# Kernel tuning notes

Hardware: AMD Instinct MI355X
Metric: run time of the kernel (lower is better)

## Reference

```python
import jax, jax.numpy as jnp
import numpy as np

B, S, D, H, ROT = 2, 2048, 2048, 16, 64
HD = D // H  # 128


def setup_inputs() -> dict:
    key = jax.random.key(0)
    ks = jax.random.split(key, 6)
    sc = 0.02
    return {
        "hidden_states": jax.random.normal(ks[0], (B, S, D), jnp.float32),
        "attention_mask": jnp.zeros((B, 1, 1, S), jnp.float32),  # HF additive mask; 0 == keep
        "position_ids": jnp.tile(jnp.arange(S, dtype=jnp.int32), (B, 1)),
        "Wq": jax.random.normal(ks[1], (D, D), jnp.float32) * sc,
        "Wk": jax.random.normal(ks[2], (D, D), jnp.float32) * sc,
        "Wv": jax.random.normal(ks[3], (D, D), jnp.float32) * sc,
        "Wo": jax.random.normal(ks[4], (D, D), jnp.float32) * sc,
        "norm_const": 0.5 * jnp.ones((1, H, 1, 1), jnp.float32),
    }


def _rotate_every_two(x):
    x1 = x[..., ::2]
    x2 = x[..., 1::2]
    return jnp.stack((-x2, x1), axis=-1).reshape(x.shape)


def _apply_rope(x, sin, cos):
    # x: [B,S,H,ROT]; sin/cos: [B,S,ROT//2] -> repeat_interleave(2) as in GPT-J
    sin2 = jnp.repeat(sin, 2, axis=-1)[:, :, None, :]
    cos2 = jnp.repeat(cos, 2, axis=-1)[:, :, None, :]
    return x * cos2 + _rotate_every_two(x) * sin2


def reference(hidden_states, attention_mask, position_ids, Wq, Wk, Wv, Wo, norm_const):
    # projections (nn.Linear, no bias): y = x @ W^T
    q = (hidden_states @ Wq.T).reshape(B, S, H, HD)
    k = (hidden_states @ Wk.T).reshape(B, S, H, HD)
    v = (hidden_states @ Wv.T).reshape(B, S, H, HD).transpose(0, 2, 1, 3)  # [B,H,S,HD]

    # GPT-J sinusoidal rotary on first ROT dims
    inv_freq = 1.0 / (10000.0 ** (jnp.arange(0, ROT, 2, dtype=jnp.float32) / ROT))
    ang = position_ids.astype(jnp.float32)[:, :, None] * inv_freq  # [B,S,ROT//2]
    sin, cos = jnp.sin(ang), jnp.cos(ang)
    q = jnp.concatenate([_apply_rope(q[..., :ROT], sin, cos), q[..., ROT:]], axis=-1)
    k = jnp.concatenate([_apply_rope(k[..., :ROT], sin, cos), k[..., ROT:]], axis=-1)
    q = q.transpose(0, 2, 1, 3)  # [B,H,S,HD]
    k = k.transpose(0, 2, 1, 3)

    # cosine attention: L2-normalize q and k (F.normalize, eps=1e-12)
    eps = 1e-12
    qn = q / jnp.clip(jnp.linalg.norm(q, axis=-1, keepdims=True), eps)
    kn = k / jnp.clip(jnp.linalg.norm(k, axis=-1, keepdims=True), eps)

    keep = attention_mask == 0                               # [B,1,1,S] bool
    causal = jnp.tril(jnp.ones((S, S), bool))[None, None]    # [1,1,S,S]
    # per-query count of visible keys -> value rescale with learned exponent
    counts = jnp.sum((causal & keep).astype(jnp.float32), axis=-1, keepdims=True)  # [B,1,S,1]
    expo = jax.nn.sigmoid(norm_const)                        # [1,H,1,1]
    v = v / jnp.clip(counts ** expo, 1.0)                    # [B,H,S,HD]

    keep_t = jnp.swapaxes(keep, -1, -2).astype(q.dtype)      # [B,1,S,1]
    qn = qn * keep_t
    kn = kn * keep_t
    v = v * keep_t

    attn = jnp.einsum('bhqd,bhkd->bhqk', qn, kn)             # cosine scores
    attn = jnp.where(causal, attn, 0.0)                      # causal zero-mask (no softmax)
    out = jnp.einsum('bhqk,bhkd->bhqd', attn, v)             # [B,H,S,HD]
    out = out.transpose(0, 2, 1, 3).reshape(B, S, D)
    return out @ Wo.T
```

## Files before the change

kernel.cpp:

```cpp
#include <hip/hip_runtime.h>
#include <hip/hip_bf16.h>

typedef __attribute__((ext_vector_type(8))) short bf16x8;
typedef __attribute__((ext_vector_type(4))) float f32x4;
typedef unsigned short u16;
typedef unsigned int u32;

constexpr int B = 2, S = 2048, D = 2048, H = 16, HD = 128, ROT = 64;
constexpr int NQKV = 3 * D;

__device__ __forceinline__ void gload16(const u16* g, u16* l)
{
    __builtin_amdgcn_global_load_lds((const __attribute__((address_space(1))) void*)g,
                                     (__attribute__((address_space(3))) void*)l, 16, 0, 0);
}

__device__ __forceinline__ float bf2f(u32 lo16) { return __uint_as_float(lo16 << 16); }

__global__ void cast_kernel(const float* __restrict__ in, u16* __restrict__ out, int n4)
{
    int idx = blockIdx.x * blockDim.x + threadIdx.x;
    int stride = gridDim.x * blockDim.x;
    for (int i = idx; i < n4; i += stride) {
        float4 v = ((const float4*)in)[i];
        __hip_bfloat16 a = __float2bfloat16(v.x);
        __hip_bfloat16 b = __float2bfloat16(v.y);
        __hip_bfloat16 c = __float2bfloat16(v.z);
        __hip_bfloat16 d = __float2bfloat16(v.w);
        ushort4 o;
        o.x = *(u16*)&a; o.y = *(u16*)&b; o.z = *(u16*)&c; o.w = *(u16*)&d;
        ((ushort4*)out)[i] = o;
    }
}

__global__ void prep_kernel(const float* __restrict__ mask, const int* __restrict__ pos,
                            const float* __restrict__ ncst,
                            float* __restrict__ sinb, float* __restrict__ cosb,
                            float* __restrict__ keep, float* __restrict__ expo)
{
    int gid = blockIdx.x * blockDim.x + threadIdx.x;
    int total = B * S * 32;
    if (gid < total) {
        int j = gid & 31;
        int bs = gid >> 5;
        float p = (float)pos[bs];
        float f = powf(10000.f, -(float)j / 32.f);
        float ang = p * f;
        sinb[gid] = sinf(ang);
        cosb[gid] = cosf(ang);
        if (j == 0) keep[bs] = (mask[bs] == 0.f) ? 1.f : 0.f;
    }
    if (gid < H) expo[gid] = 1.f / (1.f + expf(-ncst[gid]));
}

__global__ void counts_kernel(const float* __restrict__ keep, float* __restrict__ counts)
{
    __shared__ float part[256];
    int b = blockIdx.x, t = threadIdx.x;
    float v[8];
    float s = 0.f;
    const float* kp = keep + b * S + t * 8;
#pragma unroll
    for (int i = 0; i < 8; ++i) { s += kp[i]; v[i] = s; }
    part[t] = s;
    __syncthreads();
    float off = 0.f;
    for (int j = 0; j < t; ++j) off += part[j];
    float* cp = counts + b * S + t * 8;
#pragma unroll
    for (int i = 0; i < 8; ++i) cp[i] = off + v[i];
}

template <int BF16OUT>
__global__ __launch_bounds__(256) void gemm_bt(
    const u16* __restrict__ A, const u16* __restrict__ Bm,
    float* __restrict__ Cf, u16* __restrict__ Cb, int N, int K)
{
    __shared__ u16 As[2][128 * 64];
    __shared__ u16 Bs[2][128 * 64];
    int tid = threadIdx.x;
    int lane = tid & 63, w = tid >> 6;
    int wm = w >> 1, wn = w & 1;
    int bm = blockIdx.y, bn = blockIdx.x;
    const int l15 = lane & 15, l4 = lane >> 4;

    int srow = w * 32 + (lane >> 3);
    int scol = (lane & 7) * 8;
    const u16* gA = A + (size_t)(bm * 128 + srow) * K + scol;
    const u16* gB = Bm + (size_t)(bn * 128 + srow) * K + scol;

    f32x4 acc[4][4] = {};
    int nk = K / 64;

#pragma unroll
    for (int i = 0; i < 4; ++i) {
        gload16(gA + (size_t)i * 8 * K, &As[0][(w * 32 + i * 8) * 64]);
        gload16(gB + (size_t)i * 8 * K, &Bs[0][(w * 32 + i * 8) * 64]);
    }
    __syncthreads();

    int cur = 0;
    for (int t = 0; t < nk; ++t) {
        if (t + 1 < nk) {
            const u16* ga = gA + (size_t)(t + 1) * 64;
            const u16* gb = gB + (size_t)(t + 1) * 64;
#pragma unroll
            for (int i = 0; i < 4; ++i) {
                gload16(ga + (size_t)i * 8 * K, &As[cur ^ 1][(w * 32 + i * 8) * 64]);
                gload16(gb + (size_t)i * 8 * K, &Bs[cur ^ 1][(w * 32 + i * 8) * 64]);
            }
        }
#pragma unroll
        for (int tt = 0; tt < 2; ++tt) {
            bf16x8 a[4], b[4];
#pragma unroll
            for (int m = 0; m < 4; ++m)
                a[m] = *(const bf16x8*)(&As[cur][(wm * 64 + m * 16 + l15) * 64 + tt * 32 + l4 * 8]);
#pragma unroll
            for (int n = 0; n < 4; ++n)
                b[n] = *(const bf16x8*)(&Bs[cur][(wn * 64 + n * 16 + l15) * 64 + tt * 32 + l4 * 8]);
#pragma unroll
            for (int m = 0; m < 4; ++m)
#pragma unroll
                for (int n = 0; n < 4; ++n)
                    acc[m][n] = __builtin_amdgcn_mfma_f32_16x16x32_bf16(a[m], b[n], acc[m][n], 0, 0, 0);
        }
        __syncthreads();
        cur ^= 1;
    }

#pragma unroll
    for (int m = 0; m < 4; ++m) {
        int row = bm * 128 + wm * 64 + m * 16 + l4 * 4;
#pragma unroll
        for (int n = 0; n < 4; ++n) {
            int col = bn * 128 + wn * 64 + n * 16 + l15;
#pragma unroll
            for (int r = 0; r < 4; ++r) {
                if (BF16OUT) {
                    __hip_bfloat16 hv = __float2bfloat16(acc[m][n][r]);
                    Cb[(size_t)(row + r) * N + col] = *(u16*)&hv;
                } else {
                    Cf[(size_t)(row + r) * N + col] = acc[m][n][r];
                }
            }
        }
    }
}

__global__ void postproc_all(const u16* __restrict__ tmpb,
                             u16* __restrict__ qn, u16* __restrict__ kn, u16* __restrict__ vT,
                             const float* __restrict__ sinb, const float* __restrict__ cosb,
                             const float* __restrict__ keep, const float* __restrict__ counts,
                             const float* __restrict__ expo)
{
    int gw = (blockIdx.x * blockDim.x + threadIdx.x) >> 6;
    int lane = threadIdx.x & 63;
    if (gw >= B * S * H) return;
    int h = gw % H;
    int sb = gw / H;
    int s = sb % S;
    int b = sb / S;
    const u16* rowp = tmpb + (size_t)(b * S + s) * NQKV;
    u32 qv = *(const u32*)(rowp + h * 128 + lane * 2);
    u32 kv = *(const u32*)(rowp + D + h * 128 + lane * 2);
    u32 vv = *(const u32*)(rowp + 2 * D + h * 128 + lane * 2);
    float q0 = bf2f(qv & 0xffff), q1 = bf2f(qv >> 16);
    float k0 = bf2f(kv & 0xffff), k1 = bf2f(kv >> 16);
    float v0 = bf2f(vv & 0xffff), v1 = bf2f(vv >> 16);
    if (lane < 32) {
        float sn = sinb[(b * S + s) * 32 + lane];
        float cs = cosb[(b * S + s) * 32 + lane];
        float nq0 = q0 * cs - q1 * sn, nq1 = q1 * cs + q0 * sn;
        float nk0 = k0 * cs - k1 * sn, nk1 = k1 * cs + k0 * sn;
        q0 = nq0; q1 = nq1; k0 = nk0; k1 = nk1;
    }
    float sq = q0 * q0 + q1 * q1;
    float sk = k0 * k0 + k1 * k1;
#pragma unroll
    for (int o = 1; o < 64; o <<= 1) {
        sq += __shfl_xor(sq, o, 64);
        sk += __shfl_xor(sk, o, 64);
    }
    float kf = keep[b * S + s];
    float scq = kf / fmaxf(sqrtf(sq), 1e-12f);
    float sck = kf / fmaxf(sqrtf(sk), 1e-12f);
    float cnt = counts[b * S + s];
    float e = expo[h];
    float scv = kf / fmaxf(powf(cnt, e), 1.0f);

    __hip_bfloat16 a0 = __float2bfloat16(q0 * scq), a1 = __float2bfloat16(q1 * scq);
    __hip_bfloat16 b0 = __float2bfloat16(k0 * sck), b1 = __float2bfloat16(k1 * sck);
    __hip_bfloat16 c0 = __float2bfloat16(v0 * scv), c1 = __float2bfloat16(v1 * scv);
    size_t obase = ((size_t)(b * H + h) * S + s) * 128 + lane * 2;
    *(u32*)(qn + obase) = (u32)*(u16*)&a0 | ((u32)*(u16*)&a1 << 16);
    *(u32*)(kn + obase) = (u32)*(u16*)&b0 | ((u32)*(u16*)&b1 << 16);
    size_t vbase = ((size_t)(b * H + h) * 128) * (size_t)S + s;
    vT[vbase + (size_t)(2 * lane) * S] = *(u16*)&c0;
    vT[vbase + (size_t)(2 * lane + 1) * S] = *(u16*)&c1;
}

__global__ __launch_bounds__(256) void chunk_state(
    const u16* __restrict__ kn, const u16* __restrict__ vT, u16* __restrict__ T16)
{
    __shared__ u16 As[128][72];
    __shared__ u16 Bs[128][72];
    int tid = threadIdx.x, lane = tid & 63, w = tid >> 6;
    int wm = w >> 1, wn = w & 1;
    int c = blockIdx.x, bh = blockIdx.y;
    const int l15 = lane & 15, l4 = lane >> 4;
    size_t vbase = (size_t)bh * 128 * S;
    size_t kbase = (size_t)bh * S * 128;
    f32x4 acc[4][4] = {};

    for (int t = 0; t < 2; ++t) {
#pragma unroll
        for (int i = 0; i < 4; ++i) {
            int q = tid + i * 256;
            int r = q >> 3, c8 = q & 7;
            uint4 v = *(const uint4*)(vT + vbase + (size_t)r * S + c * 128 + t * 64 + c8 * 8);
            *(uint4*)(&As[r][c8 * 8]) = v;
        }
#pragma unroll
        for (int i = 0; i < 4; ++i) {
            int q = tid + i * 256;
            int r = q >> 4, c16 = q & 15;
            uint4 v = *(const uint4*)(kn + kbase + (size_t)(c * 128 + t * 64 + r) * 128 + c16 * 8);
            const u16* pv = (const u16*)&v;
#pragma unroll
            for (int j = 0; j < 8; ++j) Bs[c16 * 8 + j][r] = pv[j];
        }
        __syncthreads();
#pragma unroll
        for (int tt = 0; tt < 2; ++tt) {
            bf16x8 a[4], b[4];
#pragma unroll
            for (int m = 0; m < 4; ++m)
                a[m] = *(const bf16x8*)(&As[wm * 64 + m * 16 + l15][tt * 32 + l4 * 8]);
#pragma unroll
            for (int n = 0; n < 4; ++n)
                b[n] = *(const bf16x8*)(&Bs[wn * 64 + n * 16 + l15][tt * 32 + l4 * 8]);
#pragma unroll
            for (int m = 0; m < 4; ++m)
#pragma unroll
                for (int n = 0; n < 4; ++n)
                    acc[m][n] = __builtin_amdgcn_mfma_f32_16x16x32_bf16(a[m], b[n], acc[m][n], 0, 0, 0);
        }
        __syncthreads();
    }
#pragma unroll
    for (int m = 0; m < 4; ++m) {
        int row = wm * 64 + m * 16 + l4 * 4;
#pragma unroll
        for (int n = 0; n < 4; ++n) {
            int col = wn * 64 + n * 16 + l15;
#pragma unroll
            for (int r = 0; r < 4; ++r) {
                __hip_bfloat16 hv = __float2bfloat16(acc[m][n][r]);
                T16[((size_t)(bh * 16 + c) * 128 + row + r) * 128 + col] = *(u16*)&hv;
            }
        }
    }
}

__global__ void prefix_state(const u16* __restrict__ T16, u16* __restrict__ P16)
{
    int g = blockIdx.x * blockDim.x + threadIdx.x;
    int bh = g >> 11;
    int i8 = (g & 2047) * 8;
    const u16* tp = T16 + (size_t)bh * 16 * 16384 + i8;
    u16* pp = P16 + (size_t)bh * 16 * 16384 + i8;
    float run[8] = {};
    for (int c = 0; c < 16; ++c) {
        u16 ob[8];
#pragma unroll
        for (int j = 0; j < 8; ++j) { __hip_bfloat16 hv = __float2bfloat16(run[j]); ob[j] = *(u16*)&hv; }
        *(uint4*)(pp + (size_t)c * 16384) = *(uint4*)ob;
        uint4 tv = *(const uint4*)(tp + (size_t)c * 16384);
        const u16* tvp = (const u16*)&tv;
#pragma unroll
        for (int j = 0; j < 8; ++j) run[j] += bf2f(tvp[j]);
    }
}

__global__ __launch_bounds__(256, 2) void attn2(
    const u16* __restrict__ qn, const u16* __restrict__ kn,
    const u16* __restrict__ vT, const u16* __restrict__ P16, u16* __restrict__ ao)
{
    __shared__ u16 KN[64][136];
    __shared__ u16 VT[128][72];
    __shared__ u16 SC[128][72];
    int tid = threadIdx.x, lane = tid & 63, w = tid >> 6;
    int c = blockIdx.x, bh = blockIdx.y;
    int b = bh >> 4, h = bh & 15;
    const int l15 = lane & 15, l4 = lane >> 4;
    size_t base = (size_t)bh * S * 128;
    size_t vbase = (size_t)bh * 128 * S;
    const u16* Pp = P16 + (size_t)(bh * 16 + c) * 16384;

    bf16x8 qa[2][4];
#pragma unroll
    for (int m = 0; m < 2; ++m)
#pragma unroll
        for (int t = 0; t < 4; ++t) {
            int row = c * 128 + w * 32 + m * 16 + l15;
            qa[m][t] = *(const bf16x8*)(qn + base + (size_t)row * 128 + t * 32 + l4 * 8);
        }

    f32x4 acc[2][8] = {};

#pragma unroll
    for (int pt = 0; pt < 2; ++pt) {
#pragma unroll
        for (int i = 0; i < 4; ++i) {
            int q = tid + i * 256;
            int r = q >> 3, c8 = q & 7;
            uint4 v = *(const uint4*)(Pp + (size_t)r * 128 + pt * 64 + c8 * 8);
            *(uint4*)(&VT[r][c8 * 8]) = v;
        }
        __syncthreads();
#pragma unroll
        for (int tt = 0; tt < 2; ++tt) {
            bf16x8 pb[8];
#pragma unroll
            for (int n = 0; n < 8; ++n)
                pb[n] = *(const bf16x8*)(&VT[n * 16 + l15][tt * 32 + l4 * 8]);
#pragma unroll
            for (int m = 0; m < 2; ++m)
#pragma unroll
                for (int n = 0; n < 8; ++n)
                    acc[m][n] = __builtin_amdgcn_mfma_f32_16x16x32_bf16(qa[m][pt * 2 + tt], pb[n], acc[m][n], 0, 0, 0);
        }
        __syncthreads();
    }

    for (int kt2 = 0; kt2 < 2; ++kt2) {
#pragma unroll
        for (int i = 0; i < 4; ++i) {
            int q = tid + i * 256;
            int r = q >> 4, c8 = q & 15;
            uint4 v = *(const uint4*)(kn + base + (size_t)(c * 128 + kt2 * 64 + r) * 128 + c8 * 8);
            *(uint4*)(&KN[r][c8 * 8]) = v;
        }
#pragma unroll
        for (int i = 0; i < 4; ++i) {
            int q = tid + i * 256;
            int r = q >> 3, c8 = q & 7;
            uint4 v = *(const uint4*)(vT + vbase + (size_t)r * S + c * 128 + kt2 * 64 + c8 * 8);
            *(uint4*)(&VT[r][c8 * 8]) = v;
        }
        __syncthreads();
        f32x4 sacc[2][4] = {};
#pragma unroll
        for (int t = 0; t < 4; ++t) {
            bf16x8 kb[4];
#pragma unroll
            for (int n = 0; n < 4; ++n)
                kb[n] = *(const bf16x8*)(&KN[n * 16 + l15][t * 32 + l4 * 8]);
#pragma unroll
            for (int m = 0; m < 2; ++m)
#pragma unroll
                for (int n = 0; n < 4; ++n)
                    sacc[m][n] = __builtin_amdgcn_mfma_f32_16x16x32_bf16(qa[m][t], kb[n], sacc[m][n], 0, 0, 0);
        }
#pragma unroll
        for (int m = 0; m < 2; ++m)
#pragma unroll
            for (int n = 0; n < 4; ++n)
#pragma unroll
                for (int r = 0; r < 4; ++r) {
                    int rowl = w * 32 + m * 16 + l4 * 4 + r;
                    int coll = n * 16 + l15;
                    int kl = kt2 * 64 + coll;
                    float val = (kl <= rowl) ? sacc[m][n][r] : 0.f;
                    __hip_bfloat16 hv = __float2bfloat16(val);
                    SC[rowl][coll] = *(u16*)&hv;
                }
#pragma unroll
        for (int t = 0; t < 2; ++t) {
            bf16x8 sa[2], vb[8];
#pragma unroll
            for (int m = 0; m < 2; ++m)
                sa[m] = *(const bf16x8*)(&SC[w * 32 + m * 16 + l15][t * 32 + l4 * 8]);
#pragma unroll
            for (int n = 0; n < 8; ++n)
                vb[n] = *(const bf16x8*)(&VT[n * 16 + l15][t * 32 + l4 * 8]);
#pragma unroll
            for (int m = 0; m < 2; ++m)
#pragma unroll
                for (int n = 0; n < 8; ++n)
                    acc[m][n] = __builtin_amdgcn_mfma_f32_16x16x32_bf16(sa[m], vb[n], acc[m][n], 0, 0, 0);
        }
        __syncthreads();
    }

#pragma unroll
    for (int m = 0; m < 2; ++m)
#pragma unroll
        for (int n = 0; n < 8; ++n)
#pragma unroll
            for (int r = 0; r < 4; ++r) {
                int srow = c * 128 + w * 32 + m * 16 + l4 * 4 + r;
                int d = n * 16 + l15;
                __hip_bfloat16 hv = __float2bfloat16(acc[m][n][r]);
                ao[(size_t)(b * S + srow) * D + h * 128 + d] = *(u16*)&hv;
            }
}

extern "C" void kernel_launch(void* const* d_in, const int* in_sizes, int n_in,
                              void* d_out, int out_size, void* d_ws, size_t ws_size,
                              hipStream_t stream)
{
    const float* hs = (const float*)d_in[0];
    const float* mask = (const float*)d_in[1];
    const int* pos = (const int*)d_in[2];
    const float* Wq = (const float*)d_in[3];
    const float* Wk = (const float*)d_in[4];
    const float* Wv = (const float*)d_in[5];
    const float* Wo = (const float*)d_in[6];
    const float* ncst = (const float*)d_in[7];
    float* out = (float*)d_out;

    char* ws = (char*)d_ws;
    size_t off = 0;
    auto alloc = [&](size_t bytes) {
        size_t o = off;
        off += (bytes + 255) & ~(size_t)255;
        return o;
    };
    u16* hs16 = (u16*)(ws + alloc((size_t)B * S * D * 2));
    u16* wqkv16 = (u16*)(ws + alloc((size_t)NQKV * D * 2));
    u16* wo16 = (u16*)(ws + alloc((size_t)D * D * 2));
    u16* tmpb = (u16*)(ws + alloc((size_t)B * S * NQKV * 2));
    u16* qn16 = (u16*)(ws + alloc((size_t)B * S * D * 2));
    u16* kn16 = (u16*)(ws + alloc((size_t)B * S * D * 2));
    u16* vT16 = (u16*)(ws + alloc((size_t)B * S * D * 2));
    float* sinb = (float*)(ws + alloc((size_t)B * S * 32 * 4));
    float* cosb = (float*)(ws + alloc((size_t)B * S * 32 * 4));
    float* keep = (float*)(ws + alloc((size_t)B * S * 4));
    float* counts = (float*)(ws + alloc((size_t)B * S * 4));
    float* expo = (float*)(ws + alloc(64));
    u16* ao16 = tmpb;
    u16* T16 = tmpb + (size_t)8388608;
    u16* P16 = tmpb + (size_t)16777216;

    cast_kernel<<<2048, 256, 0, stream>>>(hs, hs16, B * S * D / 4);
    cast_kernel<<<1024, 256, 0, stream>>>(Wq, wqkv16, D * D / 4);
    cast_kernel<<<1024, 256, 0, stream>>>(Wk, wqkv16 + (size_t)D * D, D * D / 4);
    cast_kernel<<<1024, 256, 0, stream>>>(Wv, wqkv16 + (size_t)2 * D * D, D * D / 4);
    cast_kernel<<<1024, 256, 0, stream>>>(Wo, wo16, D * D / 4);
    prep_kernel<<<(B * S * 32 + 255) / 256, 256, 0, stream>>>(mask, pos, ncst, sinb, cosb, keep, expo);
    counts_kernel<<<B, 256, 0, stream>>>(keep, counts);

    dim3 gqkv(NQKV / 128, (B * S) / 128);
    gemm_bt<1><<<gqkv, 256, 0, stream>>>(hs16, wqkv16, nullptr, tmpb, NQKV, D);

    postproc_all<<<(B * S * H) / 4, 256, 0, stream>>>(tmpb, qn16, kn16, vT16, sinb, cosb, keep, counts, expo);

    dim3 gc(S / 128, B * H);
    chunk_state<<<gc, 256, 0, stream>>>(kn16, vT16, T16);
    prefix_state<<<256, 256, 0, stream>>>(T16, P16);
    attn2<<<gc, 256, 0, stream>>>(qn16, kn16, vT16, P16, ao16);

    dim3 go(D / 128, (B * S) / 128);
    gemm_bt<0><<<go, 256, 0, stream>>>(ao16, wo16, out, nullptr, D, D);
}
```

Measured before the change: 315.9 us.

## Replace GEMM with 256x256-tile 8-wave pipelined kernel and fuse weight casts

Replaces the 128x128 four-wave GEMM with a 256x256 tile, 512-thread kernel. It uses XOR-swizzled LDS, splits each K step into four phases that interleave global-to-LDS staging with MFMA work, adds setprio hints, and remaps block IDs for XCD locality. The four separate weight cast launches become one 2D-grid launch. Larger tiles raise arithmetic intensity and cut launch overhead, but they also raise register and LDS pressure. The QKV GEMM grid is now 384 blocks and the output GEMM only 128 blocks, which may underfill the 256 CUs.

```diff
diff --git a/kernel.cpp b/kernel.cpp
--- a/kernel.cpp
+++ b/kernel.cpp
@@ -33,6 +33,28 @@
     }
 }
 
+__global__ void castw_kernel(const float* __restrict__ w0, const float* __restrict__ w1,
+                             const float* __restrict__ w2, const float* __restrict__ w3,
+                             u16* __restrict__ o0, u16* __restrict__ o1,
+                             u16* __restrict__ o2, u16* __restrict__ o3, int n4)
+{
+    int which = blockIdx.y;
+    const float* src = which == 0 ? w0 : which == 1 ? w1 : which == 2 ? w2 : w3;
+    u16* dst = which == 0 ? o0 : which == 1 ? o1 : which == 2 ? o2 : o3;
+    int idx = blockIdx.x * blockDim.x + threadIdx.x;
+    int stride = gridDim.x * blockDim.x;
+    for (int i = idx; i < n4; i += stride) {
+        float4 v = ((const float4*)src)[i];
+        __hip_bfloat16 a = __float2bfloat16(v.x);
+        __hip_bfloat16 b = __float2bfloat16(v.y);
+        __hip_bfloat16 c = __float2bfloat16(v.z);
+        __hip_bfloat16 d = __float2bfloat16(v.w);
+        ushort4 o;
+        o.x = *(u16*)&a; o.y = *(u16*)&b; o.z = *(u16*)&c; o.w = *(u16*)&d;
+        ((ushort4*)dst)[i] = o;
+    }
+}
+
 __global__ void prep_kernel(const float* __restrict__ mask, const int* __restrict__ pos,
                             const float* __restrict__ ncst,
                             float* __restrict__ sinb, float* __restrict__ cosb,
@@ -71,70 +93,123 @@
     for (int i = 0; i < 8; ++i) cp[i] = off + v[i];
 }
 
+
+__device__ __forceinline__ void stage_half(const u16* __restrict__ G, int ldk,
+                                           int trow0, int kt, u16* lbuf,
+                                           int half, int w, int lane)
+{
+#pragma unroll
+    for (int l = 0; l < 2; ++l) {
+        int idx = l * 512 + w * 64 + lane;
+        int row = idx >> 3;
+        int col8 = (idx & 7) ^ (row & 7);
+        const u16* g = G + (size_t)(trow0 + half * 128 + row) * ldk + kt * 64 + col8 * 8;
+        u16* ld = lbuf + half * 8192 + (size_t)(l * 512 + w * 64) * 8;
+        gload16(g, ld);
+    }
+}
+
+template <int P, bool READS_AFTER_BARRIER>
+__device__ __forceinline__ void do_phase(const u16* abuf, const u16* bbuf,
+                                         f32x4 (&acc)[8][4],
+                                         int wm, int wn, int l15, int l4)
+{
+    constexpr int MH = P >> 1, NH = P & 1;
+    if (READS_AFTER_BARRIER) __builtin_amdgcn_s_barrier();
+    bf16x8 af[4][2], bfr[2][2];
+#pragma unroll
+    for (int i = 0; i < 4; ++i) {
+        int row = wm * 128 + MH * 64 + i * 16 + l15;
+#pragma unroll
+        for (int ks = 0; ks < 2; ++ks) {
+            int slot = (ks * 4 + l4) ^ (row & 7);
+            af[i][ks] = *(const bf16x8*)(abuf + row * 64 + slot * 8);
+        }
+    }
+#pragma unroll
+    for (int j = 0; j < 2; ++j) {
+        int row = wn * 64 + NH * 32 + j * 16 + l15;
+#pragma unroll
+        for (int ks = 0; ks < 2; ++ks) {
+            int slot = (ks * 4 + l4) ^ (row & 7);
+            bfr[j][ks] = *(const bf16x8*)(bbuf + row * 64 + slot * 8);
+        }
+    }
+    if (!READS_AFTER_BARRIER) __builtin_amdgcn_s_barrier();
+    __builtin_amdgcn_s_setprio(1);
+#pragma unroll
+    for (int ks = 0; ks < 2; ++ks)
+#pragma unroll
+        for (int i = 0; i < 4; ++i)
+#pragma unroll
+            for (int j = 0; j < 2; ++j)
+                acc[MH * 4 + i][NH * 2 + j] = __builtin_amdgcn_mfma_f32_16x16x32_bf16(
+                    af[i][ks], bfr[j][ks], acc[MH * 4 + i][NH * 2 + j], 0, 0, 0);
+    __builtin_amdgcn_s_setprio(0);
+    __builtin_amdgcn_s_barrier();
+}
+
 template <int BF16OUT>
-__global__ __launch_bounds__(256) void gemm_bt(
+__global__ __launch_bounds__(512, 2) void gemm8p(
     const u16* __restrict__ A, const u16* __restrict__ Bm,
-    float* __restrict__ Cf, u16* __restrict__ Cb, int N, int K)
-{
-    __shared__ u16 As[2][128 * 64];
-    __shared__ u16 Bs[2][128 * 64];
-    int tid = threadIdx.x;
-    int lane = tid & 63, w = tid >> 6;
-    int wm = w >> 1, wn = w & 1;
-    int bm = blockIdx.y, bn = blockIdx.x;
+    float* __restrict__ Cf, u16* __restrict__ Cb, int N, int K, int ntn)
+{
+    __shared__ u16 As[2][16384];
+    __shared__ u16 Bs[2][16384];
+    const int tid = threadIdx.x;
+    const int lane = tid & 63;
+    const int w = tid >> 6;
+    const int wm = w >> 2;
+    const int wn = w & 3;
     const int l15 = lane & 15, l4 = lane >> 4;
 
-    int srow = w * 32 + (lane >> 3);
-    int scol = (lane & 7) * 8;
-    const u16* gA = A + (size_t)(bm * 128 + srow) * K + scol;
-    const u16* gB = Bm + (size_t)(bn * 128 + srow) * K + scol;
-
-    f32x4 acc[4][4] = {};
-    int nk = K / 64;
-
-#pragma unroll
-    for (int i = 0; i < 4; ++i) {
-        gload16(gA + (size_t)i * 8 * K, &As[0][(w * 32 + i * 8) * 64]);
-        gload16(gB + (size_t)i * 8 * K, &Bs[0][(w * 32 + i * 8) * 64]);
-    }
-    __syncthreads();
-
-    int cur = 0;
+    int nwg = gridDim.x;
+    int bid = blockIdx.x;
+    int cpx = nwg >> 3;
+    int sbid = (bid & 7) * cpx + (bid >> 3);
+    int bm = sbid / ntn, bn = sbid % ntn;
+    const int bmrow = bm * 256, bnrow = bn * 256;
+
+    f32x4 acc[8][4] = {};
+    const int nk = K >> 6;
+
+    stage_half(A, K, bmrow, 0, &As[0][0], 0, w, lane);
+    stage_half(A, K, bmrow, 0, &As[0][0], 1, w, lane);
+    stage_half(Bm, K, bnrow, 0, &Bs[0][0], 0, w, lane);
+    stage_half(Bm, K, bnrow, 0, &Bs[0][0], 1, w, lane);
+
     for (int t = 0; t < nk; ++t) {
-        if (t + 1 < nk) {
-            const u16* ga = gA + (size_t)(t + 1) * 64;
-            const u16* gb = gB + (size_t)(t + 1) * 64;
-#pragma unroll
-            for (int i = 0; i < 4; ++i) {
-                gload16(ga + (size_t)i * 8 * K, &As[cur ^ 1][(w * 32 + i * 8) * 64]);
-                gload16(gb + (size_t)i * 8 * K, &Bs[cur ^ 1][(w * 32 + i * 8) * 64]);
-            }
-        }
-#pragma unroll
-        for (int tt = 0; tt < 2; ++tt) {
-            bf16x8 a[4], b[4];
-#pragma unroll
-            for (int m = 0; m < 4; ++m)
-                a[m] = *(const bf16x8*)(&As[cur][(wm * 64 + m * 16 + l15) * 64 + tt * 32 + l4 * 8]);
-#pragma unroll
-            for (int n = 0; n < 4; ++n)
-                b[n] = *(const bf16x8*)(&Bs[cur][(wn * 64 + n * 16 + l15) * 64 + tt * 32 + l4 * 8]);
-#pragma unroll
-            for (int m = 0; m < 4; ++m)
-#pragma unroll
-                for (int n = 0; n < 4; ++n)
-                    acc[m][n] = __builtin_amdgcn_mfma_f32_16x16x32_bf16(a[m], b[n], acc[m][n], 0, 0, 0);
-        }
-        __syncthreads();
-        cur ^= 1;
-    }
-
-#pragma unroll
-    for (int m = 0; m < 4; ++m) {
-        int row = bm * 128 + wm * 64 + m * 16 + l4 * 4;
+        const u16* ab = &As[t & 1][0];
+        const u16* bb = &Bs[t & 1][0];
+        u16* an = &As[(t + 1) & 1][0];
+        u16* bn2 = &Bs[(t + 1) & 1][0];
+        const bool pf = (t + 1 < nk);
+
+        if (pf) {
+            stage_half(A, K, bmrow, t + 1, an, 0, w, lane);
+            asm volatile("s_waitcnt vmcnt(2)" ::: "memory");
+        } else {
+            asm volatile("s_waitcnt vmcnt(0)" ::: "memory");
+        }
+        __builtin_amdgcn_sched_barrier(0);
+        do_phase<0, true>(ab, bb, acc, wm, wn, l15, l4);
+
+        if (pf) stage_half(A, K, bmrow, t + 1, an, 1, w, lane);
+        do_phase<1, false>(ab, bb, acc, wm, wn, l15, l4);
+
+        if (pf) stage_half(Bm, K, bnrow, t + 1, bn2, 0, w, lane);
+        do_phase<2, false>(ab, bb, acc, wm, wn, l15, l4);
+
+        if (pf) stage_half(Bm, K, bnrow, t + 1, bn2, 1, w, lane);
+        do_phase<3, false>(ab, bb, acc, wm, wn, l15, l4);
+    }
+
+#pragma unroll
+    for (int m = 0; m < 8; ++m) {
+        int row = bmrow + wm * 128 + m * 16 + l4 * 4;
 #pragma unroll
         for (int n = 0; n < 4; ++n) {
-            int col = bn * 128 + wn * 64 + n * 16 + l15;
+            int col = bnrow + wn * 64 + n * 16 + l15;
 #pragma unroll
             for (int r = 0; r < 4; ++r) {
                 if (BF16OUT) {
@@ -445,15 +520,14 @@
     u16* P16 = tmpb + (size_t)16777216;
 
     cast_kernel<<<2048, 256, 0, stream>>>(hs, hs16, B * S * D / 4);
-    cast_kernel<<<1024, 256, 0, stream>>>(Wq, wqkv16, D * D / 4);
-    cast_kernel<<<1024, 256, 0, stream>>>(Wk, wqkv16 + (size_t)D * D, D * D / 4);
-    cast_kernel<<<1024, 256, 0, stream>>>(Wv, wqkv16 + (size_t)2 * D * D, D * D / 4);
-    cast_kernel<<<1024, 256, 0, stream>>>(Wo, wo16, D * D / 4);
+    castw_kernel<<<dim3(512, 4), 256, 0, stream>>>(
+        Wq, Wk, Wv, Wo,
+        wqkv16, wqkv16 + (size_t)D * D, wqkv16 + (size_t)2 * D * D, wo16, D * D / 4);
     prep_kernel<<<(B * S * 32 + 255) / 256, 256, 0, stream>>>(mask, pos, ncst, sinb, cosb, keep, expo);
     counts_kernel<<<B, 256, 0, stream>>>(keep, counts);
 
-    dim3 gqkv(NQKV / 128, (B * S) / 128);
-    gemm_bt<1><<<gqkv, 256, 0, stream>>>(hs16, wqkv16, nullptr, tmpb, NQKV, D);
+    gemm8p<1><<<(4096 / 256) * (NQKV / 256), 512, 0, stream>>>(
+        hs16, wqkv16, nullptr, tmpb, NQKV, D, NQKV / 256);
 
     postproc_all<<<(B * S * H) / 4, 256, 0, stream>>>(tmpb, qn16, kn16, vT16, sinb, cosb, keep, counts, expo);
 
@@ -462,6 +536,6 @@
     prefix_state<<<256, 256, 0, stream>>>(T16, P16);
     attn2<<<gc, 256, 0, stream>>>(qn16, kn16, vT16, P16, ao16);
 
-    dim3 go(D / 128, (B * S) / 128);
-    gemm_bt<0><<<go, 256, 0, stream>>>(ao16, wo16, out, nullptr, D, D);
-}
+    gemm8p<0><<<(4096 / 256) * (D / 256), 512, 0, stream>>>(
+        ao16, wo16, out, nullptr, D, D, D / 256);
+}
```

Result: slower. 436.1 us (+38.1%).
